# Kernel optimization log

Hardware: AMD Instinct MI355X
Metric: run time of the kernel (lower is better)

Reference implementation:

```python
import jax, jax.numpy as jnp
import numpy as np

B, L, H = 8, 2048, 1024
Q_END = 63  # question_ends


def setup_inputs() -> dict:
    key = jax.random.key(0)
    k1, k2 = jax.random.split(key)
    encoder_out = jax.random.normal(k1, (B, L, H), dtype=jnp.float32)
    # simW: nn.Linear(3H, 1, bias=False) -> weight vector of length 3H
    w = jax.random.normal(k2, (3 * H,), dtype=jnp.float32) * (1.0 / np.sqrt(3 * H))
    return {"encoder_out": encoder_out, "w": w, "question_ends": Q_END}


def reference(encoder_out, w, question_ends):
    h = encoder_out.shape[-1]
    j_len = question_ends + 1  # static python int
    query = encoder_out[:, :j_len, :]    # (B, J, H)
    context = encoder_out[:, j_len:, :]  # (B, T, H)
    # Decompose simW(cat(c, q, c*q)) = c.w_c + q.w_q + sum_h c_h q_h w_m_h
    w_c, w_q, w_m = w[:h], w[h:2 * h], w[2 * h:]
    c_term = context @ w_c               # (B, T)
    q_term = query @ w_q                 # (B, J)
    cross = jnp.einsum('bth,bjh->btj', context * w_m, query)  # (B, T, J)
    S = c_term[:, :, None] + q_term[:, None, :] + cross        # (B, T, J)
    # context-to-query attention
    c2q = jnp.einsum('btj,bjh->bth', jax.nn.softmax(S, axis=-1), query)  # (B, T, H)
    # query-to-context attention
    b_att = jax.nn.softmax(jnp.max(S, axis=2), axis=-1)  # (B, T)
    q2c = jnp.einsum('bt,bth->bh', b_att, context)[:, None, :]  # (B, 1, H), broadcasts over T
    G = jnp.concatenate(
        [context, c2q, context * c2q, context * q2c], axis=-1)  # (B, T, 4H)
    return (query, G)
```

## Files before the change

### kernel.cpp

```cpp
#include <hip/hip_runtime.h>
#include <math.h>

#define BB 8
#define LL 2048
#define HH 1024
#define JL 64
#define TT 1984
#define NT2 62

#define QT_OFF   0
#define PQ_OFF   (QT_OFF + BB*JL)
#define PDEN_OFF (PQ_OFF + BB*NT2*HH)
#define PMAX_OFF (PDEN_OFF + 512)
#define Q2C_OFF  (PMAX_OFF + 512)
#define QTR_OFF  (Q2C_OFF + BB*HH)
#define PWS_OFF  (QTR_OFF + BB*HH*JL/2)

typedef __attribute__((ext_vector_type(8))) short bf16x8;
typedef __attribute__((ext_vector_type(4))) float f32x4;

__device__ inline ushort f2bf(float x) {
  uint u = __float_as_uint(x);
  return (ushort)((u + 0x7FFFu + ((u >> 16) & 1u)) >> 16);
}

__device__ inline void nt_store4(float* p, float a, float b2, float c, float d) {
  f32x4 v = {a, b2, c, d};
  __builtin_nontemporal_store(v, (f32x4*)p);
}

__global__ __launch_bounds__(256) void k0(const float* __restrict__ enc,
                                          const float* __restrict__ w,
                                          float* __restrict__ out,
                                          float* __restrict__ ws) {
  int j = blockIdx.x, b = blockIdx.y, tid = threadIdx.x;
  const float* qrow = enc + ((size_t)b*LL + j)*HH;
  float4 v = *(const float4*)(qrow + tid*4);
  *(float4*)(out + ((size_t)b*JL + j)*HH + tid*4) = v;
  ushort* qT = (ushort*)(ws + QTR_OFF) + (size_t)b*HH*JL + j;
  qT[(size_t)(tid*4+0)*JL] = f2bf(v.x);
  qT[(size_t)(tid*4+1)*JL] = f2bf(v.y);
  qT[(size_t)(tid*4+2)*JL] = f2bf(v.z);
  qT[(size_t)(tid*4+3)*JL] = f2bf(v.w);
  float4 wq = *(const float4*)(w + HH + tid*4);
  float a = v.x*wq.x + v.y*wq.y + v.z*wq.z + v.w*wq.w;
  #pragma unroll
  for (int o = 32; o > 0; o >>= 1) a += __shfl_xor(a, o);
  __shared__ float red[4];
  if ((tid & 63) == 0) red[tid >> 6] = a;
  __syncthreads();
  if (tid == 0) ws[QT_OFF + b*JL + j] = red[0]+red[1]+red[2]+red[3];
}

__global__ __launch_bounds__(256) void kA(const float* __restrict__ enc,
                                          const float* __restrict__ w,
                                          float* __restrict__ ws) {
  __shared__ ushort ctx_s[32][72];
  __shared__ ushort qm_s[64][72];
  __shared__ ushort P_s[32][72];
  __shared__ float mpart[32][2];
  __shared__ float spart[32][2];
  __shared__ float m_s[32];
  __shared__ float w_s[32];
  const int b = blockIdx.y, bx = blockIdx.x;
  const int t0 = bx * 32;
  const int tid = threadIdx.x;
  const int lane = tid & 63, wvi = tid >> 6;
  const int fr = lane & 15, fg = lane >> 4;
  const int mrow = (wvi & 1) * 16;
  const int nhalf = wvi >> 1;
  const float* ctx = enc + ((size_t)b*LL + JL)*HH;
  const float* qry = enc + (size_t)b*LL*HH;
  const float* wc = w;
  const float* wm = w + 2*HH;
  f32x4 acc[2];
  acc[0] = (f32x4){0.f,0.f,0.f,0.f};
  acc[1] = (f32x4){0.f,0.f,0.f,0.f};
  for (int h0 = 0; h0 < HH; h0 += 64) {
    #pragma unroll
    for (int it = 0; it < 2; ++it) {
      int idx = it*256 + tid;
      int r = idx >> 4, c4 = idx & 15;
      float4 cv = *(const float4*)(ctx + (size_t)(t0 + r)*HH + h0 + c4*4);
      *(ushort4*)&ctx_s[r][c4*4] =
          make_ushort4(f2bf(cv.x), f2bf(cv.y), f2bf(cv.z), f2bf(cv.w));
    }
    #pragma unroll
    for (int it = 0; it < 4; ++it) {
      int idx = it*256 + tid;
      int r = idx >> 4, c4 = idx & 15;
      float4 qv = *(const float4*)(qry + (size_t)r*HH + h0 + c4*4);
      float4 mv = *(const float4*)(wm + h0 + c4*4);
      float4 wvv = *(const float4*)(wc + h0 + c4*4);
      *(ushort4*)&qm_s[r][c4*4] =
          make_ushort4(f2bf(qv.x*mv.x + wvv.x), f2bf(qv.y*mv.y + wvv.y),
                       f2bf(qv.z*mv.z + wvv.z), f2bf(qv.w*mv.w + wvv.w));
    }
    __syncthreads();
    #pragma unroll
    for (int kk = 0; kk < 2; ++kk) {
      bf16x8 a = *(const bf16x8*)&ctx_s[mrow + fr][kk*32 + fg*8];
      #pragma unroll
      for (int nf = 0; nf < 2; ++nf) {
        bf16x8 bb = *(const bf16x8*)&qm_s[nhalf*32 + nf*16 + fr][kk*32 + fg*8];
        acc[nf] = __builtin_amdgcn_mfma_f32_16x16x32_bf16(a, bb, acc[nf], 0, 0, 0);
      }
    }
    __syncthreads();
  }
  float qt0 = ws[QT_OFF + (size_t)b*JL + nhalf*32 + fr];
  float qt1 = ws[QT_OFF + (size_t)b*JL + nhalf*32 + 16 + fr];
  float s0r[4], s1r[4], e0r[4], e1r[4], mr[4];
  #pragma unroll
  for (int r = 0; r < 4; ++r) {
    s0r[r] = acc[0][r] + qt0;
    s1r[r] = acc[1][r] + qt1;
    float pm = fmaxf(s0r[r], s1r[r]);
    #pragma unroll
    for (int o = 1; o < 16; o <<= 1) pm = fmaxf(pm, __shfl_xor(pm, o));
    if (fr == 0) mpart[mrow + fg*4 + r][nhalf] = pm;
  }
  __syncthreads();
  #pragma unroll
  for (int r = 0; r < 4; ++r) {
    const int row = mrow + fg*4 + r;
    float m = fmaxf(mpart[row][0], mpart[row][1]);
    mr[r] = m;
    e0r[r] = __expf(s0r[r] - m);
    e1r[r] = __expf(s1r[r] - m);
    float ps = e0r[r] + e1r[r];
    #pragma unroll
    for (int o = 1; o < 16; o <<= 1) ps += __shfl_xor(ps, o);
    if (fr == 0) spart[row][nhalf] = ps;
  }
  __syncthreads();
  #pragma unroll
  for (int r = 0; r < 4; ++r) {
    const int row = mrow + fg*4 + r;
    float inv = 1.f / (spart[row][0] + spart[row][1]);
    P_s[row][nhalf*32 +      fr] = f2bf(e0r[r]*inv);
    P_s[row][nhalf*32 + 16 + fr] = f2bf(e1r[r]*inv);
    if (fr == 0 && nhalf == 0) m_s[row] = mr[r];
  }
  __syncthreads();
  if (tid < 32) {
    float mv2 = m_s[tid];
    float M = mv2;
    #pragma unroll
    for (int o = 1; o < 32; o <<= 1) M = fmaxf(M, __shfl_xor(M, o));
    float wv2 = __expf(mv2 - M);
    w_s[tid] = wv2;
    float den = wv2;
    #pragma unroll
    for (int o = 1; o < 32; o <<= 1) den += __shfl_xor(den, o);
    if (tid == 0) {
      ws[PDEN_OFF + b*NT2 + bx] = den;
      ws[PMAX_OFF + b*NT2 + bx] = M;
    }
  }
  __syncthreads();
  {
    ushort* Pb = (ushort*)(ws + PWS_OFF) + ((size_t)b*TT + t0)*JL;
    int row = tid >> 3, g = tid & 7;
    *(uint4*)(Pb + (size_t)row*JL + g*8) = *(const uint4*)&P_s[row][g*8];
  }
  {
    const int hc = tid * 4;
    const float* ctxb = ctx + (size_t)t0*HH + hc;
    float4 a0 = {0,0,0,0}, a1 = {0,0,0,0};
    #pragma unroll 8
    for (int t = 0; t < 32; t += 2) {
      float w0 = w_s[t], w1 = w_s[t+1];
      float4 v0 = *(const float4*)(ctxb + (size_t)t*HH);
      float4 v1 = *(const float4*)(ctxb + (size_t)(t+1)*HH);
      a0.x += w0*v0.x; a0.y += w0*v0.y; a0.z += w0*v0.z; a0.w += w0*v0.w;
      a1.x += w1*v1.x; a1.y += w1*v1.y; a1.z += w1*v1.z; a1.w += w1*v1.w;
    }
    a0.x += a1.x; a0.y += a1.y; a0.z += a1.z; a0.w += a1.w;
    *(float4*)(ws + PQ_OFF + ((size_t)(b*NT2 + bx))*HH + hc) = a0;
  }
}

__global__ __launch_bounds__(256) void k2(float* __restrict__ ws) {
  int b = blockIdx.x, tid = threadIdx.x;
  float M = -1e30f;
  #pragma unroll
  for (int c = 0; c < NT2; ++c) M = fmaxf(M, ws[PMAX_OFF + b*NT2 + c]);
  float den = 0.f;
  #pragma unroll
  for (int c = 0; c < NT2; ++c)
    den += __expf(ws[PMAX_OFF + b*NT2 + c] - M) * ws[PDEN_OFF + b*NT2 + c];
  float inv = 1.f / den;
  float4 a = {0,0,0,0};
  for (int c = 0; c < NT2; ++c) {
    float e = __expf(ws[PMAX_OFF + b*NT2 + c] - M);
    float4 v = *(const float4*)(ws + PQ_OFF + ((size_t)(b*NT2 + c))*HH + tid*4);
    a.x += e*v.x; a.y += e*v.y; a.z += e*v.z; a.w += e*v.w;
  }
  a.x *= inv; a.y *= inv; a.z *= inv; a.w *= inv;
  *(float4*)(ws + Q2C_OFF + (size_t)b*HH + tid*4) = a;
}

__global__ __launch_bounds__(256) void kB(const float* __restrict__ enc,
                                          const float* __restrict__ ws,
                                          float* __restrict__ out) {
  __shared__ ushort P_s[16][72];
  __shared__ float c2q_s[2][16][260];
  const int b = blockIdx.y, t0 = blockIdx.x*16, tid = threadIdx.x;
  const int lane = tid & 63, wvi = tid >> 6;
  const int fr = lane & 15, fg = lane >> 4;
  const ushort* Pb = (const ushort*)(ws + PWS_OFF) + ((size_t)b*TT + t0)*JL;
  if (tid < 128) {
    int row = tid >> 3, g = tid & 7;
    *(uint4*)&P_s[row][g*8] = *(const uint4*)(Pb + (size_t)row*JL + g*8);
  }
  const ushort* qTg = (const ushort*)(ws + QTR_OFF) + (size_t)b*HH*JL;
  const float* ctx = enc + ((size_t)b*LL + JL)*HH;
  float* G = out + (size_t)BB*JL*HH + (size_t)b*TT*4096;
  const int hl = lane * 4;
  __syncthreads();
  for (int ch = 0; ch < 4; ++ch) {
    const int h0 = ch * 256;
    const int cur = ch & 1;
    float4 ctxr[4];
    #pragma unroll
    for (int p = 0; p < 4; ++p)
      ctxr[p] = *(const float4*)(ctx + (size_t)(t0 + p*4 + wvi)*HH + h0 + hl);
    float4 qcr = *(const float4*)(ws + Q2C_OFF + (size_t)b*HH + h0 + hl);
    f32x4 acc2[4];
    #pragma unroll
    for (int hh = 0; hh < 4; ++hh) acc2[hh] = (f32x4){0.f,0.f,0.f,0.f};
    #pragma unroll
    for (int hh = 0; hh < 4; ++hh) {
      #pragma unroll
      for (int kk = 0; kk < 2; ++kk) {
        bf16x8 a = *(const bf16x8*)(qTg + (size_t)(h0 + wvi*64 + hh*16 + fr)*JL + kk*32 + fg*8);
        bf16x8 bb = *(const bf16x8*)&P_s[fr][kk*32 + fg*8];
        acc2[hh] = __builtin_amdgcn_mfma_f32_16x16x32_bf16(a, bb, acc2[hh], 0, 0, 0);
      }
    }
    #pragma unroll
    for (int hh = 0; hh < 4; ++hh)
      *(f32x4*)&c2q_s[cur][fr][wvi*64 + hh*16 + fg*4] = acc2[hh];
    __syncthreads();
    #pragma unroll
    for (int p = 0; p < 4; ++p) {
      const int t = p*4 + wvi;
      float4 c2 = *(const float4*)&c2q_s[cur][t][hl];
      float4 cv = ctxr[p];
      float* Gr = G + (size_t)(t0 + t)*4096 + h0 + hl;
      nt_store4(Gr,        cv.x, cv.y, cv.z, cv.w);
      nt_store4(Gr + 1024, c2.x, c2.y, c2.z, c2.w);
      nt_store4(Gr + 2048, cv.x*c2.x, cv.y*c2.y, cv.z*c2.z, cv.w*c2.w);
      nt_store4(Gr + 3072, cv.x*qcr.x, cv.y*qcr.y, cv.z*qcr.z, cv.w*qcr.w);
    }
  }
}

extern "C" void kernel_launch(void* const* d_in, const int* in_sizes, int n_in,
                              void* d_out, int out_size, void* d_ws, size_t ws_size,
                              hipStream_t stream) {
  const float* enc = (const float*)d_in[0];
  const float* w   = (const float*)d_in[1];
  float* out = (float*)d_out;
  float* ws  = (float*)d_ws;
  k0<<<dim3(JL, BB), 256, 0, stream>>>(enc, w, out, ws);
  kA<<<dim3(NT2, BB), 256, 0, stream>>>(enc, w, ws);
  k2<<<BB, 256, 0, stream>>>(ws);
  kB<<<dim3(TT/16, BB), 256, 0, stream>>>(enc, ws, out);
}
```

Before: 110.4 us.

## Fuse score/softmax with c2q output pass, split q2c term into trailing kernel

Merges the score/softmax kernel and the c2q/G-writing kernel into one kernel over 16-row tiles. The softmax probabilities stay in shared memory instead of going through a global workspace round-trip, and only the last G quarter (context*q2c), which needs the global q2c reduction, moves into a new light kernel k3. The query*w_m + w_c bf16 operand is now precomputed once in k0 instead of being rebuilt in every score block. The cost is that k3 rereads the context, and there are twice as many partial q2c blocks for k2 to reduce.

```diff
diff --git a/kernel.cpp b/kernel.cpp
--- a/kernel.cpp
+++ b/kernel.cpp
@@ -6,15 +6,15 @@
 #define HH 1024
 #define JL 64
 #define TT 1984
-#define NT2 62
+#define NT3 124
 
 #define QT_OFF   0
-#define PQ_OFF   (QT_OFF + BB*JL)
-#define PDEN_OFF (PQ_OFF + BB*NT2*HH)
-#define PMAX_OFF (PDEN_OFF + 512)
-#define Q2C_OFF  (PMAX_OFF + 512)
+#define PQ_OFF   (QT_OFF + 512)
+#define PDEN_OFF (PQ_OFF + BB*NT3*HH)
+#define PMAX_OFF (PDEN_OFF + 1024)
+#define Q2C_OFF  (PMAX_OFF + 1024)
 #define QTR_OFF  (Q2C_OFF + BB*HH)
-#define PWS_OFF  (QTR_OFF + BB*HH*JL/2)
+#define QM_OFF   (QTR_OFF + BB*HH*JL/2)
 
 typedef __attribute__((ext_vector_type(8))) short bf16x8;
 typedef __attribute__((ext_vector_type(4))) float f32x4;
@@ -42,6 +42,11 @@
   qT[(size_t)(tid*4+1)*JL] = f2bf(v.y);
   qT[(size_t)(tid*4+2)*JL] = f2bf(v.z);
   qT[(size_t)(tid*4+3)*JL] = f2bf(v.w);
+  float4 wmv = *(const float4*)(w + 2*HH + tid*4);
+  float4 wcv = *(const float4*)(w + tid*4);
+  ushort* qm = (ushort*)(ws + QM_OFF) + ((size_t)b*JL + j)*HH + tid*4;
+  *(ushort4*)qm = make_ushort4(f2bf(v.x*wmv.x + wcv.x), f2bf(v.y*wmv.y + wcv.y),
+                               f2bf(v.z*wmv.z + wcv.z), f2bf(v.w*wmv.w + wcv.w));
   float4 wq = *(const float4*)(w + HH + tid*4);
   float a = v.x*wq.x + v.y*wq.y + v.z*wq.z + v.w*wq.w;
   #pragma unroll
@@ -52,181 +57,110 @@
   if (tid == 0) ws[QT_OFF + b*JL + j] = red[0]+red[1]+red[2]+red[3];
 }
 
-__global__ __launch_bounds__(256) void kA(const float* __restrict__ enc,
-                                          const float* __restrict__ w,
-                                          float* __restrict__ ws) {
-  __shared__ ushort ctx_s[32][72];
+__global__ __launch_bounds__(256) void kF(const float* __restrict__ enc,
+                                          float* __restrict__ ws,
+                                          float* __restrict__ out) {
+  __shared__ ushort ctx_s[16][72];
   __shared__ ushort qm_s[64][72];
-  __shared__ ushort P_s[32][72];
-  __shared__ float mpart[32][2];
-  __shared__ float spart[32][2];
-  __shared__ float m_s[32];
-  __shared__ float w_s[32];
+  __shared__ ushort P_s[16][72];
+  __shared__ float c2q_s[16][260];
+  __shared__ float mpart[16][4], spart[16][4];
+  __shared__ float m_s[16], w_s[16];
   const int b = blockIdx.y, bx = blockIdx.x;
-  const int t0 = bx * 32;
+  const int t0 = bx * 16;
   const int tid = threadIdx.x;
   const int lane = tid & 63, wvi = tid >> 6;
   const int fr = lane & 15, fg = lane >> 4;
-  const int mrow = (wvi & 1) * 16;
-  const int nhalf = wvi >> 1;
   const float* ctx = enc + ((size_t)b*LL + JL)*HH;
-  const float* qry = enc + (size_t)b*LL*HH;
-  const float* wc = w;
-  const float* wm = w + 2*HH;
-  f32x4 acc[2];
-  acc[0] = (f32x4){0.f,0.f,0.f,0.f};
-  acc[1] = (f32x4){0.f,0.f,0.f,0.f};
+  const ushort* qmg = (const ushort*)(ws + QM_OFF) + (size_t)b*JL*HH;
+  f32x4 accS = (f32x4){0.f,0.f,0.f,0.f};
+  const int srow = tid >> 4, sc4 = tid & 15;
+  const int qrow = tid >> 2, qseg = (tid & 3)*16;
   for (int h0 = 0; h0 < HH; h0 += 64) {
-    #pragma unroll
-    for (int it = 0; it < 2; ++it) {
-      int idx = it*256 + tid;
-      int r = idx >> 4, c4 = idx & 15;
-      float4 cv = *(const float4*)(ctx + (size_t)(t0 + r)*HH + h0 + c4*4);
-      *(ushort4*)&ctx_s[r][c4*4] =
-          make_ushort4(f2bf(cv.x), f2bf(cv.y), f2bf(cv.z), f2bf(cv.w));
-    }
-    #pragma unroll
-    for (int it = 0; it < 4; ++it) {
-      int idx = it*256 + tid;
-      int r = idx >> 4, c4 = idx & 15;
-      float4 qv = *(const float4*)(qry + (size_t)r*HH + h0 + c4*4);
-      float4 mv = *(const float4*)(wm + h0 + c4*4);
-      float4 wvv = *(const float4*)(wc + h0 + c4*4);
-      *(ushort4*)&qm_s[r][c4*4] =
-          make_ushort4(f2bf(qv.x*mv.x + wvv.x), f2bf(qv.y*mv.y + wvv.y),
-                       f2bf(qv.z*mv.z + wvv.z), f2bf(qv.w*mv.w + wvv.w));
-    }
+    float4 cv = *(const float4*)(ctx + (size_t)(t0 + srow)*HH + h0 + sc4*4);
+    *(ushort4*)&ctx_s[srow][sc4*4] =
+        make_ushort4(f2bf(cv.x), f2bf(cv.y), f2bf(cv.z), f2bf(cv.w));
+    const ushort* qg = qmg + (size_t)qrow*HH + h0 + qseg;
+    *(uint4*)&qm_s[qrow][qseg]     = *(const uint4*)(qg);
+    *(uint4*)&qm_s[qrow][qseg + 8] = *(const uint4*)(qg + 8);
     __syncthreads();
     #pragma unroll
     for (int kk = 0; kk < 2; ++kk) {
-      bf16x8 a = *(const bf16x8*)&ctx_s[mrow + fr][kk*32 + fg*8];
-      #pragma unroll
-      for (int nf = 0; nf < 2; ++nf) {
-        bf16x8 bb = *(const bf16x8*)&qm_s[nhalf*32 + nf*16 + fr][kk*32 + fg*8];
-        acc[nf] = __builtin_amdgcn_mfma_f32_16x16x32_bf16(a, bb, acc[nf], 0, 0, 0);
-      }
-    }
-    __syncthreads();
-  }
-  float qt0 = ws[QT_OFF + (size_t)b*JL + nhalf*32 + fr];
-  float qt1 = ws[QT_OFF + (size_t)b*JL + nhalf*32 + 16 + fr];
-  float s0r[4], s1r[4], e0r[4], e1r[4], mr[4];
+      bf16x8 a = *(const bf16x8*)&ctx_s[fr][kk*32 + fg*8];
+      bf16x8 bb = *(const bf16x8*)&qm_s[wvi*16 + fr][kk*32 + fg*8];
+      accS = __builtin_amdgcn_mfma_f32_16x16x32_bf16(a, bb, accS, 0, 0, 0);
+    }
+    __syncthreads();
+  }
+  const float qt = ws[QT_OFF + (size_t)b*JL + wvi*16 + fr];
+  float sv[4], ev[4], mrr[4];
   #pragma unroll
   for (int r = 0; r < 4; ++r) {
-    s0r[r] = acc[0][r] + qt0;
-    s1r[r] = acc[1][r] + qt1;
-    float pm = fmaxf(s0r[r], s1r[r]);
+    sv[r] = accS[r] + qt;
+    float pm = sv[r];
     #pragma unroll
     for (int o = 1; o < 16; o <<= 1) pm = fmaxf(pm, __shfl_xor(pm, o));
-    if (fr == 0) mpart[mrow + fg*4 + r][nhalf] = pm;
+    if (fr == 0) mpart[fg*4 + r][wvi] = pm;
   }
   __syncthreads();
   #pragma unroll
   for (int r = 0; r < 4; ++r) {
-    const int row = mrow + fg*4 + r;
-    float m = fmaxf(mpart[row][0], mpart[row][1]);
-    mr[r] = m;
-    e0r[r] = __expf(s0r[r] - m);
-    e1r[r] = __expf(s1r[r] - m);
-    float ps = e0r[r] + e1r[r];
+    const int row = fg*4 + r;
+    float m = fmaxf(fmaxf(mpart[row][0], mpart[row][1]),
+                    fmaxf(mpart[row][2], mpart[row][3]));
+    mrr[r] = m;
+    ev[r] = __expf(sv[r] - m);
+    float ps = ev[r];
     #pragma unroll
     for (int o = 1; o < 16; o <<= 1) ps += __shfl_xor(ps, o);
-    if (fr == 0) spart[row][nhalf] = ps;
+    if (fr == 0) spart[row][wvi] = ps;
   }
   __syncthreads();
   #pragma unroll
   for (int r = 0; r < 4; ++r) {
-    const int row = mrow + fg*4 + r;
-    float inv = 1.f / (spart[row][0] + spart[row][1]);
-    P_s[row][nhalf*32 +      fr] = f2bf(e0r[r]*inv);
-    P_s[row][nhalf*32 + 16 + fr] = f2bf(e1r[r]*inv);
-    if (fr == 0 && nhalf == 0) m_s[row] = mr[r];
-  }
-  __syncthreads();
-  if (tid < 32) {
+    const int row = fg*4 + r;
+    float inv = 1.f / (spart[row][0] + spart[row][1] + spart[row][2] + spart[row][3]);
+    P_s[row][wvi*16 + fr] = f2bf(ev[r]*inv);
+    if (fr == 0 && wvi == 0) m_s[row] = mrr[r];
+  }
+  __syncthreads();
+  if (tid < 16) {
     float mv2 = m_s[tid];
     float M = mv2;
     #pragma unroll
-    for (int o = 1; o < 32; o <<= 1) M = fmaxf(M, __shfl_xor(M, o));
+    for (int o = 1; o < 16; o <<= 1) M = fmaxf(M, __shfl_xor(M, o));
     float wv2 = __expf(mv2 - M);
     w_s[tid] = wv2;
     float den = wv2;
     #pragma unroll
-    for (int o = 1; o < 32; o <<= 1) den += __shfl_xor(den, o);
+    for (int o = 1; o < 16; o <<= 1) den += __shfl_xor(den, o);
     if (tid == 0) {
-      ws[PDEN_OFF + b*NT2 + bx] = den;
-      ws[PMAX_OFF + b*NT2 + bx] = M;
-    }
-  }
-  __syncthreads();
-  {
-    ushort* Pb = (ushort*)(ws + PWS_OFF) + ((size_t)b*TT + t0)*JL;
-    int row = tid >> 3, g = tid & 7;
-    *(uint4*)(Pb + (size_t)row*JL + g*8) = *(const uint4*)&P_s[row][g*8];
-  }
+      ws[PDEN_OFF + b*NT3 + bx] = den;
+      ws[PMAX_OFF + b*NT3 + bx] = M;
+    }
+  }
+  __syncthreads();
   {
     const int hc = tid * 4;
     const float* ctxb = ctx + (size_t)t0*HH + hc;
-    float4 a0 = {0,0,0,0}, a1 = {0,0,0,0};
-    #pragma unroll 8
-    for (int t = 0; t < 32; t += 2) {
-      float w0 = w_s[t], w1 = w_s[t+1];
+    float4 a0 = {0,0,0,0};
+    #pragma unroll
+    for (int t = 0; t < 16; ++t) {
+      float w0 = w_s[t];
       float4 v0 = *(const float4*)(ctxb + (size_t)t*HH);
-      float4 v1 = *(const float4*)(ctxb + (size_t)(t+1)*HH);
       a0.x += w0*v0.x; a0.y += w0*v0.y; a0.z += w0*v0.z; a0.w += w0*v0.w;
-      a1.x += w1*v1.x; a1.y += w1*v1.y; a1.z += w1*v1.z; a1.w += w1*v1.w;
-    }
-    a0.x += a1.x; a0.y += a1.y; a0.z += a1.z; a0.w += a1.w;
-    *(float4*)(ws + PQ_OFF + ((size_t)(b*NT2 + bx))*HH + hc) = a0;
-  }
-}
-
-__global__ __launch_bounds__(256) void k2(float* __restrict__ ws) {
-  int b = blockIdx.x, tid = threadIdx.x;
-  float M = -1e30f;
-  #pragma unroll
-  for (int c = 0; c < NT2; ++c) M = fmaxf(M, ws[PMAX_OFF + b*NT2 + c]);
-  float den = 0.f;
-  #pragma unroll
-  for (int c = 0; c < NT2; ++c)
-    den += __expf(ws[PMAX_OFF + b*NT2 + c] - M) * ws[PDEN_OFF + b*NT2 + c];
-  float inv = 1.f / den;
-  float4 a = {0,0,0,0};
-  for (int c = 0; c < NT2; ++c) {
-    float e = __expf(ws[PMAX_OFF + b*NT2 + c] - M);
-    float4 v = *(const float4*)(ws + PQ_OFF + ((size_t)(b*NT2 + c))*HH + tid*4);
-    a.x += e*v.x; a.y += e*v.y; a.z += e*v.z; a.w += e*v.w;
-  }
-  a.x *= inv; a.y *= inv; a.z *= inv; a.w *= inv;
-  *(float4*)(ws + Q2C_OFF + (size_t)b*HH + tid*4) = a;
-}
-
-__global__ __launch_bounds__(256) void kB(const float* __restrict__ enc,
-                                          const float* __restrict__ ws,
-                                          float* __restrict__ out) {
-  __shared__ ushort P_s[16][72];
-  __shared__ float c2q_s[2][16][260];
-  const int b = blockIdx.y, t0 = blockIdx.x*16, tid = threadIdx.x;
-  const int lane = tid & 63, wvi = tid >> 6;
-  const int fr = lane & 15, fg = lane >> 4;
-  const ushort* Pb = (const ushort*)(ws + PWS_OFF) + ((size_t)b*TT + t0)*JL;
-  if (tid < 128) {
-    int row = tid >> 3, g = tid & 7;
-    *(uint4*)&P_s[row][g*8] = *(const uint4*)(Pb + (size_t)row*JL + g*8);
+    }
+    *(float4*)(ws + PQ_OFF + ((size_t)(b*NT3 + bx))*HH + hc) = a0;
   }
   const ushort* qTg = (const ushort*)(ws + QTR_OFF) + (size_t)b*HH*JL;
-  const float* ctx = enc + ((size_t)b*LL + JL)*HH;
   float* G = out + (size_t)BB*JL*HH + (size_t)b*TT*4096;
   const int hl = lane * 4;
-  __syncthreads();
   for (int ch = 0; ch < 4; ++ch) {
     const int h0 = ch * 256;
-    const int cur = ch & 1;
     float4 ctxr[4];
     #pragma unroll
     for (int p = 0; p < 4; ++p)
       ctxr[p] = *(const float4*)(ctx + (size_t)(t0 + p*4 + wvi)*HH + h0 + hl);
-    float4 qcr = *(const float4*)(ws + Q2C_OFF + (size_t)b*HH + h0 + hl);
     f32x4 acc2[4];
     #pragma unroll
     for (int hh = 0; hh < 4; ++hh) acc2[hh] = (f32x4){0.f,0.f,0.f,0.f};
@@ -241,19 +175,52 @@
     }
     #pragma unroll
     for (int hh = 0; hh < 4; ++hh)
-      *(f32x4*)&c2q_s[cur][fr][wvi*64 + hh*16 + fg*4] = acc2[hh];
+      *(f32x4*)&c2q_s[fr][wvi*64 + hh*16 + fg*4] = acc2[hh];
     __syncthreads();
     #pragma unroll
     for (int p = 0; p < 4; ++p) {
       const int t = p*4 + wvi;
-      float4 c2 = *(const float4*)&c2q_s[cur][t][hl];
+      float4 c2 = *(const float4*)&c2q_s[t][hl];
       float4 cv = ctxr[p];
       float* Gr = G + (size_t)(t0 + t)*4096 + h0 + hl;
       nt_store4(Gr,        cv.x, cv.y, cv.z, cv.w);
       nt_store4(Gr + 1024, c2.x, c2.y, c2.z, c2.w);
       nt_store4(Gr + 2048, cv.x*c2.x, cv.y*c2.y, cv.z*c2.z, cv.w*c2.w);
-      nt_store4(Gr + 3072, cv.x*qcr.x, cv.y*qcr.y, cv.z*qcr.z, cv.w*qcr.w);
-    }
+    }
+    __syncthreads();
+  }
+}
+
+__global__ __launch_bounds__(256) void k2(float* __restrict__ ws) {
+  int b = blockIdx.x, tid = threadIdx.x;
+  float M = -1e30f;
+  for (int c = 0; c < NT3; ++c) M = fmaxf(M, ws[PMAX_OFF + b*NT3 + c]);
+  float den = 0.f;
+  for (int c = 0; c < NT3; ++c)
+    den += __expf(ws[PMAX_OFF + b*NT3 + c] - M) * ws[PDEN_OFF + b*NT3 + c];
+  float inv = 1.f / den;
+  float4 a = {0,0,0,0};
+  for (int c = 0; c < NT3; ++c) {
+    float e = __expf(ws[PMAX_OFF + b*NT3 + c] - M);
+    float4 v = *(const float4*)(ws + PQ_OFF + ((size_t)(b*NT3 + c))*HH + tid*4);
+    a.x += e*v.x; a.y += e*v.y; a.z += e*v.z; a.w += e*v.w;
+  }
+  a.x *= inv; a.y *= inv; a.z *= inv; a.w *= inv;
+  *(float4*)(ws + Q2C_OFF + (size_t)b*HH + tid*4) = a;
+}
+
+__global__ __launch_bounds__(256) void k3(const float* __restrict__ enc,
+                                          const float* __restrict__ ws,
+                                          float* __restrict__ out) {
+  const int b = blockIdx.y, t0 = blockIdx.x*16, tid = threadIdx.x;
+  float4 qc = *(const float4*)(ws + Q2C_OFF + (size_t)b*HH + tid*4);
+  const float* ctx = enc + ((size_t)b*LL + JL + t0)*HH;
+  float* G = out + (size_t)BB*JL*HH + ((size_t)b*TT + t0)*4096;
+  #pragma unroll
+  for (int rr = 0; rr < 16; ++rr) {
+    float4 cv = *(const float4*)(ctx + (size_t)rr*HH + tid*4);
+    nt_store4(G + (size_t)rr*4096 + 3072 + tid*4,
+              cv.x*qc.x, cv.y*qc.y, cv.z*qc.z, cv.w*qc.w);
   }
 }
 
@@ -265,7 +232,7 @@
   float* out = (float*)d_out;
   float* ws  = (float*)d_ws;
   k0<<<dim3(JL, BB), 256, 0, stream>>>(enc, w, out, ws);
-  kA<<<dim3(NT2, BB), 256, 0, stream>>>(enc, w, ws);
+  kF<<<dim3(NT3, BB), 256, 0, stream>>>(enc, ws, out);
   k2<<<BB, 256, 0, stream>>>(ws);
-  kB<<<dim3(TT/16, BB), 256, 0, stream>>>(enc, ws, out);
-}
+  k3<<<dim3(NT3, BB), 256, 0, stream>>>(enc, ws, out);
+}
```

Result: slower. 116.1 us (+5.2%).
